# Optimization experiments

Measured on AMD Instinct MI355X. Metric: run time of the kernel, lower is better.

## Reference

```python
import jax, jax.numpy as jnp
import numpy as np

T, B = 110, 256            # max_seq_len, num dialogues (all length T)
N = T * B                  # total graph nodes
DM = 300                   # fused input dim (100 text + 100 audio + 100 visual)
F = 200                    # 2*D_e node feature dim
H = 64                     # graph_hidden_size
R = 8                      # num relations (2 speakers x 2 speakers x 2 directions)
NB = 30                    # RGCN num_bases
NC = 7                     # n_classes
DA = F + H                 # matchatt / classifier input dim
WP, WF = 10, 10            # window_past, window_future

def _build_edges():
    src, dst = [], []
    for j in range(T):
        for i in range(max(0, j - WP), min(T, j + WF + 1)):
            src.append(j); dst.append(i)
    return np.asarray(src, np.int32), np.asarray(dst, np.int32)

SRC_T, DST_T = _build_edges()                    # per-dialogue edge endpoints [E0]
DIRN = (SRC_T >= DST_T).astype(np.int32)         # direction bit: '0' iff j < i
OFF = np.arange(B, dtype=np.int32) * T
SRC = (OFF[:, None] + SRC_T[None, :]).reshape(-1)  # global src node ids, dialogue-major
DST = (OFF[:, None] + DST_T[None, :]).reshape(-1)
E = SRC.shape[0]

def _p(key, shape, scale=0.05):
    return (jax.random.normal(key, shape) * scale).astype(jnp.float32)

def setup_inputs():
    key = jax.random.key(0)
    ks = jax.random.split(key, 16)
    return {
        "textf": jax.random.normal(ks[0], (T, B, 100), jnp.float32),
        "acouf": jax.random.normal(ks[1], (T, B, 100), jnp.float32),
        "visuf": jax.random.normal(ks[2], (T, B, 100), jnp.float32),
        "speakers": jax.random.randint(ks[3], (T, B), 0, 2, jnp.int32),
        "Wf": _p(ks[4], (DM, F)), "bf": jnp.zeros((F,), jnp.float32),
        "basis": _p(ks[5], (NB, F, H)), "comp": _p(ks[6], (R, NB)),
        "root": _p(ks[7], (F, H)), "b_rgcn": jnp.zeros((H,), jnp.float32),
        "Wrel": _p(ks[8], (H, H)), "brel": jnp.zeros((H,), jnp.float32),
        "Wroot2": _p(ks[9], (H, H)),
        "Wma": _p(ks[10], (DA, DA)), "bma": jnp.zeros((DA,), jnp.float32),
        "Wl": _p(ks[11], (DA, H)), "bl": jnp.zeros((H,), jnp.float32),
        "Ws": _p(ks[12], (H, NC)), "bs": jnp.zeros((NC,), jnp.float32),
    }

def reference(textf, acouf, visuf, speakers, Wf, bf, basis, comp, root, b_rgcn,
              Wrel, brel, Wroot2, Wma, bma, Wl, bl, Ws, bs):
    src, dst = jnp.asarray(SRC), jnp.asarray(DST)
    # feature fusion: concat modalities -> linear, [T,B,300] -> [T,B,200]
    feats = jnp.concatenate([textf, acouf, visuf], axis=-1) @ Wf + bf
    x = jnp.transpose(feats, (1, 0, 2)).reshape(N, F)       # node features, dialogue-major
    # edge types from speaker ids: key '{s0}{s1}{dir}' -> s0*4 + s1*2 + dir
    s0 = speakers[SRC_T]                                    # [E0, B]
    s1 = speakers[DST_T]
    et = (s0 * 4 + s1 * 2 + jnp.asarray(DIRN)[:, None]).T.reshape(-1)  # [E]
    # --- RGCNConv (basis decomposition, per-relation mean aggregation) ---
    Wrels = jnp.einsum('rb,bfh->rfh', comp, basis)          # [R,F,H]
    xr = jnp.einsum('nf,rfh->nrh', x, Wrels)                # [N,R,H] projected per relation
    msg = xr[src, et]                                       # [E,H] gather
    seg = dst * R + et
    summ = jax.ops.segment_sum(msg, seg, num_segments=N * R).reshape(N, R, H)
    cnt = jax.ops.segment_sum(jnp.ones((E,), jnp.float32), seg, num_segments=N * R).reshape(N, R, 1)
    h1 = (summ / jnp.maximum(cnt, 1.0)).sum(1) + x @ root + b_rgcn   # [N,H]
    # --- GraphConv (sum aggregation) ---
    agg = jax.ops.segment_sum(h1[src], dst, num_segments=N)
    h2 = agg @ Wrel + brel + h1 @ Wroot2                    # [N,H]
    emotions = jnp.concatenate([x, h2], axis=-1)            # [N,DA]
    # --- nodal MatchingAttention ('general2') over full equal-length dialogues ---
    M = emotions.reshape(B, T, DA).transpose(1, 0, 2)       # [T,B,DA]
    umask = jnp.ones((B, T), jnp.float32)
    Xq = M @ Wma + bma                                      # [T,B,DA] transformed queries
    scores = jnp.einsum('tbd,sbd->tbs', Xq, M * umask.T[:, :, None])
    scores = jnp.tanh(scores * umask[None])
    alpha = jax.nn.softmax(scores, axis=-1) * umask[None]
    alpha = alpha / alpha.sum(-1, keepdims=True)
    att = jnp.einsum('tbs,sbd->tbd', alpha, M)              # [T,B,DA]
    hidden = jax.nn.relu(att @ Wl + bl)                     # dropout = identity (eval)
    logits = hidden @ Ws + bs
    logp = jax.nn.log_softmax(logits, axis=-1)              # [T,B,NC]
    # unpad/concat per dialogue (all lengths == T) -> [B*T, NC]
    return jnp.transpose(logp, (1, 0, 2)).reshape(N, NC)
```

## Files before the change

kernel.cpp:

```cpp
#include <hip/hip_runtime.h>

#define TT   110
#define BBD  256
#define NND  28160
#define WIN  10

typedef __bf16 bf16x8 __attribute__((ext_vector_type(8)));
typedef __bf16 bf16x4 __attribute__((ext_vector_type(4)));
typedef float  f32x4  __attribute__((ext_vector_type(4)));

__device__ __forceinline__ int imax(int a, int b){ return a > b ? a : b; }
__device__ __forceinline__ int imin(int a, int b){ return a < b ? a : b; }


__global__ __launch_bounds__(256) void wrels_k(
    const float* __restrict__ basis, const float* __restrict__ comp,
    const float* __restrict__ root, float* __restrict__ wrels)
{
  int idx = blockIdx.x * 256 + threadIdx.x;
  if (idx >= 115200) return;
  int r = idx / 12800, fh = idx % 12800;
  float v;
  if (r < 8) {
    v = 0.f;
    #pragma unroll
    for (int nb = 0; nb < 30; ++nb) v += comp[r*30 + nb] * basis[nb*12800 + fh];
  } else {
    v = root[fh];
  }
  wrels[idx] = v;
}

__global__ __launch_bounds__(256) void prep_k(
    const float* __restrict__ textf, const float* __restrict__ acouf,
    const float* __restrict__ visuf, const float* __restrict__ wrels,
    const float* __restrict__ Wf, const float* __restrict__ Wma,
    const float* __restrict__ Wl, const float* __restrict__ Wrel,
    const float* __restrict__ Wroot2, __bf16* __restrict__ Ain,
    __bf16* __restrict__ img)
{
  constexpr int T0 = 1126400;
  constexpr int T1 = T0 + 10240;
  constexpr int T2 = T1 + 18432;
  constexpr int T3 = T2 + 12800;
  constexpr int T4 = T3 + 2560;
  constexpr int T5 = T4 + 1024;
  for (int c = blockIdx.x * 256 + threadIdx.x; c < T5; c += gridDim.x * 256) {
    bf16x8 v;
    __bf16* dst;
    if (c < T0) {
      const int m = c / 40, cc = c - m * 40;
      const int col0 = cc << 3;
      const size_t ab = (size_t)m * 100;
      #pragma unroll
      for (int e = 0; e < 8; ++e) {
        const int col = col0 + e;
        float x = (col < 100) ? textf[ab + col]
                : (col < 200) ? acouf[ab + col - 100]
                : (col < 300) ? visuf[ab + col - 200] : 0.f;
        v[e] = (__bf16)x;
      }
      dst = Ain + (size_t)m * 320 + col0;
    } else if (c < T1) {
      const int r = c - T0;
      const int cb = r / 2560, r2 = r - cb * 2560;
      const int col = r2 / 40, ch = r2 - col * 40;
      const int cs = (ch & ~7) | ((ch ^ col) & 7);
      const int gc = (cb << 6) + col;
      #pragma unroll
      for (int e = 0; e < 8; ++e) {
        const int k = (cs << 3) + e;
        v[e] = (__bf16)((k < 300 && gc < 200) ? Wf[k*200 + gc] : 0.f);
      }
      dst = img + cb * 20480 + col * 320 + (ch << 3);
    } else if (c < T2) {
      const int r = c - T1;
      const int cb = r / 2048, r2 = r - cb * 2048;
      const int col = r2 / 32, ch = r2 - col * 32;
      const int cs = (ch & ~7) | ((ch ^ col) & 7);
      #pragma unroll
      for (int e = 0; e < 8; ++e) {
        const int k = (cs << 3) + e;
        v[e] = (__bf16)((k < 200) ? wrels[cb*12800 + k*64 + col] : 0.f);
      }
      dst = img + 81920 + cb * 16384 + col * 256 + (ch << 3);
    } else if (c < T3) {
      const int r = c - T2;
      const int cb = r / 2560, r2 = r - cb * 2560;
      const int col = r2 / 40, ch = r2 - col * 40;
      const int cs = (ch & ~7) | ((ch ^ col) & 7);
      const int gc = (cb << 6) + col;
      #pragma unroll
      for (int e = 0; e < 8; ++e) {
        const int k = (cs << 3) + e;
        v[e] = (__bf16)((k < 264 && gc < 264) ? Wma[k*264 + gc] : 0.f);
      }
      dst = img + 229376 + cb * 20480 + col * 320 + (ch << 3);
    } else if (c < T4) {
      const int r = c - T3;
      const int col = r / 40, ch = r - col * 40;
      const int cs = (ch & ~7) | ((ch ^ col) & 7);
      #pragma unroll
      for (int e = 0; e < 8; ++e) {
        const int k = (cs << 3) + e;
        v[e] = (__bf16)((k < 264) ? Wl[k*64 + col] : 0.f);
      }
      dst = img + 331776 + col * 320 + (ch << 3);
    } else {
      const int r = c - T4;
      const int col = r / 16, ch = r - col * 16;
      const int cs = (ch & ~7) | ((ch ^ col) & 7);
      #pragma unroll
      for (int e = 0; e < 8; ++e) {
        const int k = (cs << 3) + e;
        v[e] = (__bf16)((k < 64) ? Wrel[k*64 + col] : Wroot2[(k-64)*64 + col]);
      }
      dst = img + 352256 + col * 128 + (ch << 3);
    }
    *(bf16x8*)dst = v;
  }
}

template<int MODE, int NK, int KSP, int NCB, int OUT>
__global__ __launch_bounds__(256) void bgemm_k(
    const __bf16* __restrict__ A0, const __bf16* __restrict__ A1,
    const __bf16* __restrict__ Bimg, const float* __restrict__ bias,
    void* __restrict__ Cv, int Ncols, const int* __restrict__ spkm)
{
  __shared__ __align__(16) __bf16 Bsh[64][KSP];
  const int tid = threadIdx.x;
  constexpr int NWT = 440 * NCB;
  constexpr int q = NWT >> 3;
  const int bid = blockIdx.x;
  const int w = (bid & 7) * q + (bid >> 3);
  const int m0 = (w / NCB) << 6;
  const int cb = w % NCB;
  const int n0 = cb << 6;

  {
    const bf16x8* src = (const bf16x8*)(Bimg + (size_t)cb * (64 * KSP));
    bf16x8* dst = (bf16x8*)&Bsh[0][0];
    constexpr int NIT = (64 * KSP / 8) / 256;
    #pragma unroll
    for (int c = 0; c < NIT; ++c) dst[c * 256 + tid] = src[c * 256 + tid];
  }
  __syncthreads();

  const int wid = tid >> 6, lane = tid & 63;
  const int wm = wid >> 1, wn = wid & 1;
  const int fr = lane & 15;
  const int fk = (lane >> 4) << 3;
  const int row0 = (lane >> 4) << 2;

  f32x4 acc[2][2];
  #pragma unroll
  for (int f = 0; f < 2; ++f)
    #pragma unroll
    for (int g = 0; g < 2; ++g) acc[f][g] = (f32x4){0.f,0.f,0.f,0.f};

  #pragma unroll
  for (int kt = 0; kt < NK; ++kt) {
    const int ko = (kt << 5) + fk;
    bf16x8 af[2];
    #pragma unroll
    for (int f = 0; f < 2; ++f) {
      const int ra = m0 + wm*32 + f*16 + fr;
      if constexpr (MODE == 2) {
        af[f] = (ko < 200) ? *(const bf16x8*)(A0 + (size_t)ra*200 + ko)
                           : *(const bf16x8*)(A1 + (size_t)ra*64 + (ko - 200));
      } else {
        constexpr int SA = (MODE == 0) ? 320 : 200;
        af[f] = *(const bf16x8*)(A0 + (size_t)ra*SA + ko);
      }
    }
    bf16x8 bfv[2];
    #pragma unroll
    for (int g = 0; g < 2; ++g) {
      const int rb_ = wn*32 + g*16 + fr;
      bfv[g] = *(const bf16x8*)&Bsh[rb_][(((ko >> 3) ^ (rb_ & 7)) << 3)];
    }
    #pragma unroll
    for (int f = 0; f < 2; ++f)
      #pragma unroll
      for (int g = 0; g < 2; ++g)
        acc[f][g] = __builtin_amdgcn_mfma_f32_16x16x32_bf16(af[f], bfv[g], acc[f][g], 0, 0, 0);
  }

  #pragma unroll
  for (int f = 0; f < 2; ++f) {
    const int gm0 = m0 + wm*32 + f*16 + row0;
    int sp[4];
    if constexpr (MODE == 1) {
      #pragma unroll
      for (int r2 = 0; r2 < 4; ++r2) sp[r2] = spkm[gm0 + r2];
    }
    #pragma unroll
    for (int g = 0; g < 2; ++g) {
      const int col = n0 + wn*32 + g*16 + fr;
      if (col < Ncols) {
        const float bv = bias ? bias[col] : 0.f;
        #pragma unroll
        for (int r2 = 0; r2 < 4; ++r2) {
          const float v = acc[f][g][r2] + bv;
          const int gm = gm0 + r2;
          bool dow = true;
          if constexpr (MODE == 1) dow = (cb == 8) || ((cb >> 2) == sp[r2]);
          if (dow) {
            if constexpr (OUT == 1) {
              ((__bf16*)Cv)[(size_t)gm * Ncols + col] = (__bf16)v;
            } else {
              __bf16* Cb = (__bf16*)Cv;
              const size_t o = (size_t)gm * 288 + col;
              const __bf16 hi = (__bf16)v;
              Cb[o] = hi;
              Cb[(size_t)288 * NND + o] = (__bf16)(v - (float)hi);
            }
          }
        }
      }
    }
  }
}

__global__ __launch_bounds__(512) void dialog_k(
    const __bf16* __restrict__ xr, const int* __restrict__ spk,
    const float* __restrict__ brg, const __bf16* __restrict__ Wgcimg,
    const float* __restrict__ brel, __bf16* __restrict__ h2)
{
  __shared__ __align__(16) __bf16 Xsh[75][320];
  __shared__ float  h1f[65][68];
  __shared__ __align__(16) __bf16 aggbf[56][72];
  __shared__ int ssp[TT];
  __shared__ int pc[TT + 1];
  const int bid = blockIdx.x;
  const int b = bid >> 1, half = bid & 1;
  const int t0   = half ? 55 : 0;
  const int H1LO = half ? 45 : 0;
  const int XLO  = half ? 35 : 0;
  const int tid = threadIdx.x;
  if (tid < TT) ssp[tid] = spk[tid * BBD + b];
  __syncthreads();
  if (tid < 64) {
    int v = (tid < TT) ? ssp[tid] : 0;
    #pragma unroll
    for (int o = 1; o < 64; o <<= 1) { const int u = __shfl_up(v, o); if (tid >= o) v += u; }
    pc[tid + 1] = v;
    const int tot = __shfl(v, 63);
    int v2 = (tid + 64 < TT) ? ssp[tid + 64] : 0;
    #pragma unroll
    for (int o = 1; o < 64; o <<= 1) { const int u = __shfl_up(v2, o); if (tid >= o) v2 += u; }
    if (tid + 64 < TT) pc[tid + 65] = tot + v2;
    if (tid == 0) pc[0] = 0;
  }
  for (int i = tid << 3; i < 75 * 320; i += 512 << 3) {
    const int xl = i / 320, off = i - xl * 320;
    const int j = XLO + xl;
    const size_t base = ((size_t)j * BBD + b) * 576;
    const int col = (off < 256) ? ((ssp[j] << 8) + off) : (256 + off);
    *(bf16x8*)&Xsh[xl][off] = *(const bf16x8*)&xr[base + col];
  }
  __syncthreads();
  const int w8 = tid >> 6, lane = tid & 63;
  const float bias = brg[lane];
  for (int lh = w8; lh < 65; lh += 8) {
    const int t = H1LO + lh;
    const int si2 = ssp[t] << 1;
    const int jlo = imax(t - WIN, 0), jhi = imin(t + WIN, TT - 1);
    const int n1d0 = pc[t] - pc[jlo];
    const int n0d0 = (t - jlo) - n1d0;
    const int n1d1 = pc[jhi + 1] - pc[t];
    const int n0d1 = (jhi - t + 1) - n1d1;
    const float r00 = 1.f / (float)imax(n0d0, 1);
    const float r10 = 1.f / (float)imax(n1d0, 1);
    const float r01 = 1.f / (float)imax(n0d1, 1);
    const float r11 = 1.f / (float)imax(n1d1, 1);
    float a = 0.f;
    if (t >= WIN && t < TT - WIN) {
      #pragma unroll
      for (int dj = -WIN; dj <= WIN; ++dj) {
        const int j = t + dj;
        const float v = (float)Xsh[j - XLO][((si2 + ((dj >= 0) ? 1 : 0)) << 6) + lane];
        const float w = (dj >= 0) ? (ssp[j] ? r11 : r01) : (ssp[j] ? r10 : r00);
        a = fmaf(w, v, a);
      }
    } else {
      #pragma unroll
      for (int dj = -WIN; dj <= WIN; ++dj) {
        const int j = t + dj;
        const int jc = imin(imax(j, XLO), XLO + 74);
        const float v = (float)Xsh[jc - XLO][((si2 + ((dj >= 0) ? 1 : 0)) << 6) + lane];
        float w = (dj >= 0) ? (ssp[jc] ? r11 : r01) : (ssp[jc] ? r10 : r00);
        if (j < 0 || j >= TT) w = 0.f;
        a = fmaf(w, v, a);
      }
    }
    a += (float)Xsh[t - XLO][256 + lane] + bias;
    h1f[lh][lane] = a;
  }
  __syncthreads();
  for (int lt = w8; lt < 55; lt += 8) {
    const int t = t0 + lt;
    float a = 0.f;
    if (t >= WIN && t < TT - WIN) {
      #pragma unroll
      for (int dj = -WIN; dj <= WIN; ++dj)
        a += h1f[t + dj - H1LO][lane];
    } else {
      #pragma unroll
      for (int dj = -WIN; dj <= WIN; ++dj) {
        const int j = t + dj;
        const int jc = imin(imax(j, H1LO), H1LO + 64);
        const float m = ((j >= 0) && (j < TT)) ? 1.f : 0.f;
        a = fmaf(m, h1f[jc - H1LO][lane], a);
      }
    }
    aggbf[lt][lane] = (__bf16)a;
  }
  __syncthreads();
  if (w8 < 4) {
    const int wm = w8 >> 1, wn = w8 & 1;
    const int fr = lane & 15, fk = (lane >> 4) << 3, row0 = (lane >> 4) << 2;
    const int lhh = t0 - H1LO;
    f32x4 acc[2][2];
    #pragma unroll
    for (int f = 0; f < 2; ++f)
      #pragma unroll
      for (int g = 0; g < 2; ++g) acc[f][g] = (f32x4){0.f,0.f,0.f,0.f};
    #pragma unroll
    for (int kt = 0; kt < 4; ++kt) {
      const int ko = (kt << 5) + fk;
      bf16x8 af[2];
      #pragma unroll
      for (int f = 0; f < 2; ++f) {
        const int tr = wm*32 + f*16 + fr;
        if (tr < 55) {
          if (ko < 64) {
            af[f] = *(const bf16x8*)&aggbf[tr][ko];
          } else {
            const float* src = &h1f[tr + lhh][ko - 64];
            const float4 u0 = ((const float4*)src)[0];
            const float4 u1 = ((const float4*)src)[1];
            af[f] = (bf16x8){(__bf16)u0.x,(__bf16)u0.y,(__bf16)u0.z,(__bf16)u0.w,
                             (__bf16)u1.x,(__bf16)u1.y,(__bf16)u1.z,(__bf16)u1.w};
          }
        } else af[f] = (bf16x8){0,0,0,0,0,0,0,0};
      }
      bf16x8 bfv[2];
      #pragma unroll
      for (int g = 0; g < 2; ++g) {
        const int rb_ = wn*32 + g*16 + fr;
        bfv[g] = *(const bf16x8*)(Wgcimg + rb_*128 + (((ko >> 3) ^ (rb_ & 7)) << 3));
      }
      #pragma unroll
      for (int f = 0; f < 2; ++f)
        #pragma unroll
        for (int g = 0; g < 2; ++g)
          acc[f][g] = __builtin_amdgcn_mfma_f32_16x16x32_bf16(af[f], bfv[g], acc[f][g], 0, 0, 0);
    }
    #pragma unroll
    for (int g = 0; g < 2; ++g) {
      const int col = wn*32 + g*16 + fr;
      const float bv = brel[col];
      #pragma unroll
      for (int f = 0; f < 2; ++f) {
        const int tr0 = wm*32 + f*16 + row0;
        #pragma unroll
        for (int r2 = 0; r2 < 4; ++r2) {
          const int tr = tr0 + r2;
          if (tr < 55) {
            const int t = t0 + tr;
            h2[((size_t)t * BBD + b) * 64 + col] = (__bf16)(acc[f][g][r2] + bv);
          }
        }
      }
    }
  }
}

__global__ __launch_bounds__(448) void attn_fused_k(
    const __bf16* __restrict__ x, const __bf16* __restrict__ h2,
    const __bf16* __restrict__ Xq, const __bf16* __restrict__ Wlimg,
    const float* __restrict__ bl, const float* __restrict__ Wsm,
    const float* __restrict__ bsm, float* __restrict__ out)
{
  __shared__ __align__(16) __bf16 Msh [TT ][272];
  __shared__ __align__(16) __bf16 MTsh[264][136];
  __shared__ __align__(16) __bf16 Ash [112][136];
  const int b = blockIdx.x;
  const int tid = threadIdx.x;

  for (int idx = tid; idx < TT * 66; idx += 448) {
    const int s = idx / 66, c4 = idx % 66;
    const size_t node = (size_t)s * BBD + b;
    bf16x4 pk;
    if (c4 < 50) pk = *(const bf16x4*)&x [node * 200 + (c4 << 2)];
    else         pk = *(const bf16x4*)&h2[node * 64 + ((c4 - 50) << 2)];
    *(bf16x4*)&Msh[s][c4 << 2] = pk;
    const int d = c4 << 2;
    MTsh[d+0][s] = pk[0]; MTsh[d+1][s] = pk[1];
    MTsh[d+2][s] = pk[2]; MTsh[d+3][s] = pk[3];
  }
  for (int idx = tid; idx < 264 * 26; idx += 448) MTsh[idx / 26][110 + idx % 26] = (__bf16)0.f;
  for (int idx = tid; idx < 112 * 24; idx += 448) Ash[idx / 24][112 + idx % 24] = (__bf16)0.f;
  __syncthreads();

  const int wid = tid >> 6, lane = tid & 63;
  const int t0 = wid << 4;
  const int fr = lane & 15;
  const int g  = lane >> 4;
  const int fk = g << 3;
  const int row0 = g << 2;

  f32x4 sacc[7];
  #pragma unroll
  for (int st = 0; st < 7; ++st) sacc[st] = (f32x4){0.f,0.f,0.f,0.f};
  const int trow = t0 + fr;
  const size_t arow = ((size_t)(trow < TT ? trow : TT - 1) * BBD + b) * 288;
  const __bf16* XqLo = Xq + (size_t)288 * NND;
  for (int kst = 0; kst < 9; ++kst) {
    const int k0 = kst << 5;
    bf16x8 aqh = *(const bf16x8*)&Xq  [arow + k0 + fk];
    bf16x8 aql = *(const bf16x8*)&XqLo[arow + k0 + fk];
    if (kst == 8 && fk != 0) {
      aqh = (bf16x8){0,0,0,0,0,0,0,0};
      aql = (bf16x8){0,0,0,0,0,0,0,0};
    }
    #pragma unroll
    for (int st = 0; st < 7; ++st) {
      bf16x8 bq;
      if (kst < 8) bq = *(const bf16x8*)&Msh[st*16 + fr][k0 + fk];
      else bq = (fk == 0) ? *(const bf16x8*)&Msh[st*16 + fr][256]
                          : (bf16x8){0,0,0,0,0,0,0,0};
      sacc[st] = __builtin_amdgcn_mfma_f32_16x16x32_bf16(aqh, bq, sacc[st], 0, 0, 0);
      sacc[st] = __builtin_amdgcn_mfma_f32_16x16x32_bf16(aql, bq, sacc[st], 0, 0, 0);
    }
  }

  #pragma unroll
  for (int r = 0; r < 4; ++r) {
    float tv[7];
    #pragma unroll
    for (int st = 0; st < 7; ++st) {
      const float e2 = __expf(2.f * sacc[st][r]);
      tv[st] = 1.f - 2.f / (e2 + 1.f);
    }
    if (fr >= 14) tv[6] = -3.0e38f;
    float mx = fmaxf(fmaxf(fmaxf(tv[0],tv[1]), fmaxf(tv[2],tv[3])),
                     fmaxf(fmaxf(tv[4],tv[5]), tv[6]));
    #pragma unroll
    for (int o = 8; o >= 1; o >>= 1) mx = fmaxf(mx, __shfl_xor(mx, o, 16));
    float e[7], sum = 0.f;
    #pragma unroll
    for (int st = 0; st < 7; ++st) { e[st] = __expf(tv[st] - mx); sum += e[st]; }
    #pragma unroll
    for (int o = 8; o >= 1; o >>= 1) sum += __shfl_xor(sum, o, 16);
    const float inv = 1.f / sum;
    const int tr = t0 + (g << 2) + r;
    #pragma unroll
    for (int st = 0; st < 7; ++st) Ash[tr][st*16 + fr] = (__bf16)(e[st] * inv);
  }
  __syncthreads();

  __bf16 (*attsh)[272] = Msh;
  const int tr2 = t0 + (g << 2);
  for (int dt = 0; dt < 17; ++dt) {
    const int d0 = dt << 4;
    f32x4 pacc = (f32x4){0.f,0.f,0.f,0.f};
    #pragma unroll
    for (int kst = 0; kst < 4; ++kst) {
      const int k0 = kst << 5;
      const bf16x8 pa = *(const bf16x8*)&Ash [t0 + fr][k0 + fk];
      const bf16x8 pb = *(const bf16x8*)&MTsh[d0 + fr][k0 + fk];
      pacc = __builtin_amdgcn_mfma_f32_16x16x32_bf16(pa, pb, pacc, 0, 0, 0);
    }
    const int col = d0 + fr;
    if (col < 264) {
      #pragma unroll
      for (int r = 0; r < 4; ++r) {
        const int t = tr2 + r;
        if (t < TT) attsh[t][col] = (__bf16)pacc[r];
      }
    }
  }
  __syncthreads();

  float* Wssh = (float*)&MTsh[0][0];
  for (int i = tid; i < 512; i += 448) {
    const int k = i >> 3, cc = i & 7;
    Wssh[(k << 3) + cc] = (cc < 7) ? Wsm[k*7 + cc] : 0.f;
  }

  float (*hidf)[68] = (float(*)[68])&Ash[0][0];
  f32x4 hacc[4];
  #pragma unroll
  for (int gg = 0; gg < 4; ++gg) hacc[gg] = (f32x4){0.f,0.f,0.f,0.f};
  #pragma unroll
  for (int kst = 0; kst < 9; ++kst) {
    const int ko = (kst << 5) + fk;
    const int ar = t0 + fr;
    bf16x8 af;
    if (ko < 264 && ar < TT) af = *(const bf16x8*)&attsh[ar][ko];
    else af = (bf16x8){0,0,0,0,0,0,0,0};
    #pragma unroll
    for (int gg = 0; gg < 4; ++gg) {
      const int rb_ = gg*16 + fr;
      const bf16x8 bfv = *(const bf16x8*)(Wlimg + rb_*320 + (((ko >> 3) ^ (rb_ & 7)) << 3));
      hacc[gg] = __builtin_amdgcn_mfma_f32_16x16x32_bf16(af, bfv, hacc[gg], 0, 0, 0);
    }
  }
  #pragma unroll
  for (int gg = 0; gg < 4; ++gg) {
    const int col = gg*16 + fr;
    const float bv = bl[col];
    #pragma unroll
    for (int r = 0; r < 4; ++r) {
      const int row = t0 + row0 + r;
      if (row < TT) hidf[row][col] = fmaxf(hacc[gg][r] + bv, 0.f);
    }
  }
  __syncthreads();

  const int c = tid & 7;
  const float bc = (c < 7) ? bsm[c] : 0.f;
  #pragma unroll
  for (int p = 0; p < 2; ++p) {
    const int lr = p * 56 + (tid >> 3);
    if (lr < TT) {
      float lg = -3.0e38f;
      if (c < 7) {
        lg = bc;
        #pragma unroll
        for (int k = 0; k < 64; ++k) lg += hidf[lr][k] * Wssh[(k << 3) + c];
      }
      float mx = lg;
      #pragma unroll
      for (int o = 4; o >= 1; o >>= 1) mx = fmaxf(mx, __shfl_xor(mx, o, 8));
      float e = (c < 7) ? __expf(lg - mx) : 0.f;
      float sm = e;
      #pragma unroll
      for (int o = 4; o >= 1; o >>= 1) sm += __shfl_xor(sm, o, 8);
      if (c < 7) out[((size_t)b * TT + lr) * 7 + c] = lg - mx - __logf(sm);
    }
  }
}

extern "C" void kernel_launch(void* const* d_in, const int* in_sizes, int n_in,
                              void* d_out, int out_size, void* d_ws, size_t ws_size,
                              hipStream_t stream)
{
  const float* textf  = (const float*)d_in[0];
  const float* acouf  = (const float*)d_in[1];
  const float* visuf  = (const float*)d_in[2];
  const int*   spk    = (const int*)  d_in[3];
  const float* Wf     = (const float*)d_in[4];
  const float* bfv    = (const float*)d_in[5];
  const float* basis  = (const float*)d_in[6];
  const float* comp   = (const float*)d_in[7];
  const float* root   = (const float*)d_in[8];
  const float* brg    = (const float*)d_in[9];
  const float* Wrel   = (const float*)d_in[10];
  const float* brel   = (const float*)d_in[11];
  const float* Wroot2 = (const float*)d_in[12];
  const float* Wma    = (const float*)d_in[13];
  const float* bma    = (const float*)d_in[14];
  const float* Wl     = (const float*)d_in[15];
  const float* bl     = (const float*)d_in[16];
  const float* Wsm    = (const float*)d_in[17];
  const float* bsm    = (const float*)d_in[18];

  float* ws = (float*)d_ws;
  float*  wrels = ws;
  __bf16* img   = (__bf16*)(ws + 115200);
  __bf16* Ain   = (__bf16*)(ws + 295424);
  __bf16* xb    = (__bf16*)(ws + 4801024);
  __bf16* xr    = (__bf16*)(ws + 7617024);
  __bf16* h2    = (__bf16*)(ws + 15727104);
  __bf16* Xqb   = (__bf16*)(ws + 16628224);
  float*  outp  = (float*)d_out;

  __bf16* Wfimg  = img;
  __bf16* wrimg  = img + 81920;
  __bf16* Wmaimg = img + 229376;
  __bf16* Wlimg  = img + 331776;
  __bf16* Wgcimg = img + 352256;

  wrels_k<<<450, 256, 0, stream>>>(basis, comp, root, wrels);
  prep_k<<<2048, 256, 0, stream>>>(textf, acouf, visuf, wrels, Wf, Wma, Wl,
                                   Wrel, Wroot2, Ain, img);
  bgemm_k<0,10,320,4,1><<<1760, 256, 0, stream>>>(Ain, nullptr, Wfimg, bfv, xb, 200, nullptr);
  bgemm_k<1,7,256,9,1><<<3960, 256, 0, stream>>>(xb, nullptr, wrimg, nullptr, xr, 576, spk);
  dialog_k<<<512, 512, 0, stream>>>(xr, spk, brg, Wgcimg, brel, h2);
  bgemm_k<2,9,320,5,2><<<2200, 256, 0, stream>>>(xb, h2, Wmaimg, bma, Xqb, 264, nullptr);
  attn_fused_k<<<256, 448, 0, stream>>>(xb, h2, Xqb, Wlimg, bl, Wsm, bsm, outp);
}
```

Baseline: 151.7 us.

## Fuse basis composition into prep kernel and drop split-bf16 Xq precision

Removes the separate wrels kernel and computes the basis-composed relation weights directly inside prep_k while packing them into the bf16 image. It also stops storing Xq as a hi/lo bf16 pair: the GEMM writes a single bf16 output with stride 264, and the attention score MFMA loop issues one MFMA per tile instead of two. This saves a kernel launch, half the Xq write and read traffic, and half the score MFMAs. The cost is lower precision in the attention scores, and the row stride changes from 288 to 264, so the 16-byte vector loads may land on less favourable alignment.

```diff
diff --git a/kernel.cpp b/kernel.cpp
--- a/kernel.cpp
+++ b/kernel.cpp
@@ -13,27 +13,10 @@
 __device__ __forceinline__ int imin(int a, int b){ return a < b ? a : b; }
 
 
-__global__ __launch_bounds__(256) void wrels_k(
-    const float* __restrict__ basis, const float* __restrict__ comp,
-    const float* __restrict__ root, float* __restrict__ wrels)
-{
-  int idx = blockIdx.x * 256 + threadIdx.x;
-  if (idx >= 115200) return;
-  int r = idx / 12800, fh = idx % 12800;
-  float v;
-  if (r < 8) {
-    v = 0.f;
-    #pragma unroll
-    for (int nb = 0; nb < 30; ++nb) v += comp[r*30 + nb] * basis[nb*12800 + fh];
-  } else {
-    v = root[fh];
-  }
-  wrels[idx] = v;
-}
-
 __global__ __launch_bounds__(256) void prep_k(
     const float* __restrict__ textf, const float* __restrict__ acouf,
-    const float* __restrict__ visuf, const float* __restrict__ wrels,
+    const float* __restrict__ visuf, const float* __restrict__ basis,
+    const float* __restrict__ comp, const float* __restrict__ root,
     const float* __restrict__ Wf, const float* __restrict__ Wma,
     const float* __restrict__ Wl, const float* __restrict__ Wrel,
     const float* __restrict__ Wroot2, __bf16* __restrict__ Ain,
@@ -75,13 +58,28 @@
       dst = img + cb * 20480 + col * 320 + (ch << 3);
     } else if (c < T2) {
       const int r = c - T1;
-      const int cb = r / 2048, r2 = r - cb * 2048;
-      const int col = r2 / 32, ch = r2 - col * 32;
+      const int cb = r >> 11, r2 = r & 2047;
+      const int col = r2 >> 5, ch = r2 & 31;
       const int cs = (ch & ~7) | ((ch ^ col) & 7);
-      #pragma unroll
-      for (int e = 0; e < 8; ++e) {
-        const int k = (cs << 3) + e;
-        v[e] = (__bf16)((k < 200) ? wrels[cb*12800 + k*64 + col] : 0.f);
+      if (cb < 8) {
+        float acc[8] = {0.f,0.f,0.f,0.f,0.f,0.f,0.f,0.f};
+        for (int nb = 0; nb < 30; ++nb) {
+          const float cmp = comp[cb*30 + nb];
+          const float* bp = basis + nb*12800 + col;
+          #pragma unroll
+          for (int e = 0; e < 8; ++e) {
+            const int k = (cs << 3) + e;
+            if (k < 200) acc[e] = fmaf(cmp, bp[k*64], acc[e]);
+          }
+        }
+        #pragma unroll
+        for (int e = 0; e < 8; ++e) v[e] = (__bf16)acc[e];
+      } else {
+        #pragma unroll
+        for (int e = 0; e < 8; ++e) {
+          const int k = (cs << 3) + e;
+          v[e] = (__bf16)((k < 200) ? root[k*64 + col] : 0.f);
+        }
       }
       dst = img + 81920 + cb * 16384 + col * 256 + (ch << 3);
     } else if (c < T3) {
@@ -206,15 +204,7 @@
           bool dow = true;
           if constexpr (MODE == 1) dow = (cb == 8) || ((cb >> 2) == sp[r2]);
           if (dow) {
-            if constexpr (OUT == 1) {
-              ((__bf16*)Cv)[(size_t)gm * Ncols + col] = (__bf16)v;
-            } else {
-              __bf16* Cb = (__bf16*)Cv;
-              const size_t o = (size_t)gm * 288 + col;
-              const __bf16 hi = (__bf16)v;
-              Cb[o] = hi;
-              Cb[(size_t)288 * NND + o] = (__bf16)(v - (float)hi);
-            }
+            ((__bf16*)Cv)[(size_t)gm * Ncols + col] = (__bf16)v;
           }
         }
       }
@@ -415,24 +405,19 @@
   #pragma unroll
   for (int st = 0; st < 7; ++st) sacc[st] = (f32x4){0.f,0.f,0.f,0.f};
   const int trow = t0 + fr;
-  const size_t arow = ((size_t)(trow < TT ? trow : TT - 1) * BBD + b) * 288;
-  const __bf16* XqLo = Xq + (size_t)288 * NND;
+  const size_t arow = ((size_t)(trow < TT ? trow : TT - 1) * BBD + b) * 264;
   for (int kst = 0; kst < 9; ++kst) {
     const int k0 = kst << 5;
-    bf16x8 aqh = *(const bf16x8*)&Xq  [arow + k0 + fk];
-    bf16x8 aql = *(const bf16x8*)&XqLo[arow + k0 + fk];
-    if (kst == 8 && fk != 0) {
-      aqh = (bf16x8){0,0,0,0,0,0,0,0};
-      aql = (bf16x8){0,0,0,0,0,0,0,0};
-    }
+    bf16x8 aq;
+    if (kst < 8 || fk == 0) aq = *(const bf16x8*)&Xq[arow + k0 + fk];
+    else aq = (bf16x8){0,0,0,0,0,0,0,0};
     #pragma unroll
     for (int st = 0; st < 7; ++st) {
       bf16x8 bq;
       if (kst < 8) bq = *(const bf16x8*)&Msh[st*16 + fr][k0 + fk];
       else bq = (fk == 0) ? *(const bf16x8*)&Msh[st*16 + fr][256]
                           : (bf16x8){0,0,0,0,0,0,0,0};
-      sacc[st] = __builtin_amdgcn_mfma_f32_16x16x32_bf16(aqh, bq, sacc[st], 0, 0, 0);
-      sacc[st] = __builtin_amdgcn_mfma_f32_16x16x32_bf16(aql, bq, sacc[st], 0, 0, 0);
+      sacc[st] = __builtin_amdgcn_mfma_f32_16x16x32_bf16(aq, bq, sacc[st], 0, 0, 0);
     }
   }
 
@@ -569,7 +554,6 @@
   const float* bsm    = (const float*)d_in[18];
 
   float* ws = (float*)d_ws;
-  float*  wrels = ws;
   __bf16* img   = (__bf16*)(ws + 115200);
   __bf16* Ain   = (__bf16*)(ws + 295424);
   __bf16* xb    = (__bf16*)(ws + 4801024);
@@ -584,12 +568,11 @@
   __bf16* Wlimg  = img + 331776;
   __bf16* Wgcimg = img + 352256;
 
-  wrels_k<<<450, 256, 0, stream>>>(basis, comp, root, wrels);
-  prep_k<<<2048, 256, 0, stream>>>(textf, acouf, visuf, wrels, Wf, Wma, Wl,
-                                   Wrel, Wroot2, Ain, img);
+  prep_k<<<2048, 256, 0, stream>>>(textf, acouf, visuf, basis, comp, root,
+                                   Wf, Wma, Wl, Wrel, Wroot2, Ain, img);
   bgemm_k<0,10,320,4,1><<<1760, 256, 0, stream>>>(Ain, nullptr, Wfimg, bfv, xb, 200, nullptr);
   bgemm_k<1,7,256,9,1><<<3960, 256, 0, stream>>>(xb, nullptr, wrimg, nullptr, xr, 576, spk);
   dialog_k<<<512, 512, 0, stream>>>(xr, spk, brg, Wgcimg, brel, h2);
-  bgemm_k<2,9,320,5,2><<<2200, 256, 0, stream>>>(xb, h2, Wmaimg, bma, Xqb, 264, nullptr);
+  bgemm_k<2,9,320,5,1><<<2200, 256, 0, stream>>>(xb, h2, Wmaimg, bma, Xqb, 264, nullptr);
   attn_fused_k<<<256, 448, 0, stream>>>(xb, h2, Xqb, Wlimg, bl, Wsm, bsm, outp);
 }
```

Result: slower. 215.1 us (+41.8%).
